# Kernel optimization log

Hardware: AMD Instinct MI355X
Metric: run time of the kernel (lower is better)

The kernel has to match this reference:

```python
import jax, jax.numpy as jnp
import numpy as np

N = 20000      # nodes
E = 320000     # edges (before self loops)
D_IN = 256
D_H = 256
D_E = 8
NEG_SLOPE = 0.2


def setup_inputs() -> dict:
    key = jax.random.key(0)
    ks = jax.random.split(key, 12)
    x = jax.random.normal(ks[0], (N, D_IN), jnp.float32)
    edge_index = jax.random.randint(ks[1], (2, E), 0, N, dtype=jnp.int32)
    edge_attr = jax.random.normal(ks[2], (E, D_E), jnp.float32)
    batch = jnp.zeros((N,), jnp.int32)

    def gat_params(k, d_in):
        k1, k2, k3 = jax.random.split(k, 3)
        W = jax.random.normal(k1, (d_in, D_H), jnp.float32) * (1.0 / np.sqrt(d_in))
        a_s = jax.random.normal(k2, (D_H,), jnp.float32) * 0.1
        a_d = jax.random.normal(k3, (D_H,), jnp.float32) * 0.1
        b = jnp.zeros((D_H,), jnp.float32)
        return W, a_s, a_d, b

    W1, as1, ad1, b1 = gat_params(ks[3], D_IN)
    W2, as2, ad2, b2 = gat_params(ks[4], D_H)
    W3, as3, ad3, b3 = gat_params(ks[5], D_H)
    return dict(x=x, edge_index=edge_index, edge_attr=edge_attr, batch=batch,
                W1=W1, as1=as1, ad1=ad1, b1=b1,
                W2=W2, as2=as2, ad2=ad2, b2=b2,
                W3=W3, as3=as3, ad3=ad3, b3=b3)


def gat_conv(x, src, dst, W, a_src, a_dst, b):
    # PyG GATConv, heads=1: h = x W; alpha_e = leakyrelu(<h_src,a_s> + <h_dst,a_d>)
    h = x @ W                                  # [N, D_H]
    s = h @ a_src                              # [N]
    d = h @ a_dst                              # [N]
    alpha = jax.nn.leaky_relu(s[src] + d[dst], NEG_SLOPE)   # [Etot]
    n = h.shape[0]
    m = jax.ops.segment_max(alpha, dst, num_segments=n)     # per-dst max
    ex = jnp.exp(alpha - m[dst])
    denom = jax.ops.segment_sum(ex, dst, num_segments=n)
    w = ex / (denom[dst] + 1e-16)
    out = jax.ops.segment_sum(h[src] * w[:, None], dst, num_segments=n)
    return out + b


def reference(x, edge_index, edge_attr, batch,
              W1, as1, ad1, b1, W2, as2, ad2, b2, W3, as3, ad3, b3):
    # row-normalize input features (zero norms -> 1e-8)
    norms = jnp.linalg.norm(x, axis=1, keepdims=True)
    norms = jnp.where(norms == 0, 1e-8, norms)
    x = x / norms

    # add self loops once (GATConv default add_self_loops=True);
    # edge_attr is ignored since edge_dim=None in GATConv defaults.
    loop = jnp.arange(N, dtype=edge_index.dtype)
    src = jnp.concatenate([edge_index[0], loop])
    dst = jnp.concatenate([edge_index[1], loop])

    x = jax.nn.gelu(gat_conv(x, src, dst, W1, as1, ad1, b1), approximate=False)
    x = jax.nn.gelu(gat_conv(x, src, dst, W2, as2, ad2, b2), approximate=False)
    x = jax.nn.gelu(gat_conv(x, src, dst, W3, as3, ad3, b3), approximate=False)
    return x
```

## Files before the change

### kernel.cpp

```cpp
#include <hip/hip_runtime.h>
#include <math.h>

#define NN 20000
#define EE 320000
#define DD 256
#define ETOT (EE + NN)
#define EDGE_CAP 1544
#define NCHUNK ((NN + 255) / 256)

typedef __attribute__((ext_vector_type(8))) short bf8;
typedef __attribute__((ext_vector_type(4))) float f32x4;

__device__ __forceinline__ float gelu_exact(float x) {
    return 0.5f * x * (1.0f + erff(x * 0.70710678118654752f));
}

__device__ __forceinline__ unsigned short f2bf(float v) {
    unsigned u = __float_as_uint(v);
    u += 0x7fffu + ((u >> 16) & 1u);
    return (unsigned short)(u >> 16);
}
__device__ __forceinline__ float bf2f(unsigned short h) {
    return __uint_as_float(((unsigned)h) << 16);
}
__device__ __forceinline__ void split2(float v, unsigned short& hi, unsigned short& lo) {
    hi = f2bf(v);
    lo = f2bf(v - bf2f(hi));
}

__global__ __launch_bounds__(256) void norm_k(const float* __restrict__ X,
                                              unsigned short* __restrict__ Xh,
                                              unsigned short* __restrict__ Xl,
                                              float* __restrict__ sdZero,
                                              int* __restrict__ deg) {
    int t = threadIdx.x;
    int bid = blockIdx.x;
    if (t < 24) sdZero[bid * 24 + t] = 0.0f;
    if (t >= 32 && t < 36) deg[bid * 4 + (t - 32)] = 1;

    int wave = (bid * 256 + t) >> 6;
    int lane = t & 63;
    const float4 v = *(const float4*)&X[wave * DD + lane * 4];
    float ss = v.x * v.x + v.y * v.y + v.z * v.z + v.w * v.w;
    for (int off = 32; off > 0; off >>= 1) ss += __shfl_down(ss, off, 64);
    ss = __shfl(ss, 0, 64);
    float n = sqrtf(ss);
    if (n == 0.0f) n = 1e-8f;
    float inv = 1.0f / n;
    float o[4] = {v.x * inv, v.y * inv, v.z * inv, v.w * inv};
    ushort4 hv, lv;
    split2(o[0], hv.x, lv.x);
    split2(o[1], hv.y, lv.y);
    split2(o[2], hv.z, lv.z);
    split2(o[3], hv.w, lv.w);
    *(ushort4*)&Xh[wave * DD + lane * 4] = hv;
    *(ushort4*)&Xl[wave * DD + lane * 4] = lv;
}

__global__ __launch_bounds__(256) void splitw_k(const float* __restrict__ W1, const float* __restrict__ W2,
                                                const float* __restrict__ W3, unsigned short* __restrict__ Whl) {
    __shared__ float tile[64][65];
    int t = threadIdx.x;
    int k0 = blockIdx.x * 64;
    int c0 = blockIdx.y * 64;
    int z = blockIdx.z;
    const float* W = (z == 0) ? W1 : (z == 1) ? W2 : W3;
    unsigned short* Wht = Whl + (size_t)z * 2 * DD * DD;
    unsigned short* Wlt = Wht + DD * DD;
#pragma unroll
    for (int i = 0; i < 16; ++i) {
        int idx = t + i * 256;
        int r = idx >> 6, c = idx & 63;
        tile[r][c] = W[(k0 + r) * DD + c0 + c];
    }
    __syncthreads();
#pragma unroll
    for (int i = 0; i < 16; ++i) {
        int idx = t + i * 256;
        int r = idx >> 6, c = idx & 63;
        float v = tile[c][r];
        unsigned short hi, lo;
        split2(v, hi, lo);
        Wht[(c0 + r) * DD + k0 + c] = hi;
        Wlt[(c0 + r) * DD + k0 + c] = lo;
    }
}

__global__ void count_k(const int* __restrict__ ei, int* deg) {
    int e = blockIdx.x * 256 + threadIdx.x;
    if (e < EE) atomicAdd(&deg[ei[EE + e]], 1);
}

__global__ __launch_bounds__(256) void scanA_k(const int* __restrict__ deg, int* __restrict__ part) {
    __shared__ int red[256];
    int t = threadIdx.x;
    int idx = blockIdx.x * 256 + t;
    red[t] = (idx < NN) ? deg[idx] : 0;
    __syncthreads();
    for (int s = 128; s > 0; s >>= 1) {
        if (t < s) red[t] += red[t + s];
        __syncthreads();
    }
    if (t == 0) part[blockIdx.x] = red[0];
}

__global__ __launch_bounds__(128) void scanB_k(int* __restrict__ part, int* __restrict__ offs) {
    __shared__ int sh[NCHUNK];
    int t = threadIdx.x;
    if (t < NCHUNK) sh[t] = part[t];
    __syncthreads();
    if (t == 0) {
        int run = 0;
        for (int i = 0; i < NCHUNK; ++i) {
            int v = sh[i];
            sh[i] = run;
            run += v;
        }
        offs[NN] = run;
    }
    __syncthreads();
    if (t < NCHUNK) part[t] = sh[t];
}

__global__ __launch_bounds__(256) void scanC_k(const int* __restrict__ deg, const int* __restrict__ part,
                                               int* __restrict__ offs, int* __restrict__ cursor,
                                               int* __restrict__ csr, int* __restrict__ csrD) {
    __shared__ int sh[256];
    int t = threadIdx.x;
    int idx = blockIdx.x * 256 + t;
    int v = (idx < NN) ? deg[idx] : 0;
    sh[t] = v;
    __syncthreads();
    for (int s = 1; s < 256; s <<= 1) {
        int u = (t >= s) ? sh[t - s] : 0;
        __syncthreads();
        sh[t] += u;
        __syncthreads();
    }
    if (idx < NN) {
        int run = part[blockIdx.x] + sh[t] - v;
        offs[idx] = run;
        cursor[idx] = run + 1;
        csr[run] = idx;
        csrD[run] = idx;
    }
}

__global__ void fill_k(const int* __restrict__ ei, int* cursor, int* __restrict__ csr,
                       int* __restrict__ csrD) {
    int e = blockIdx.x * 256 + threadIdx.x;
    if (e < EE) {
        int s = ei[e];
        int d = ei[EE + e];
        int p = atomicAdd(&cursor[d], 1);
        csr[p] = s;
        csrD[p] = d;
    }
}

__global__ __launch_bounds__(256) void alpha_k(const float* __restrict__ sArr,
                                               const float* __restrict__ dArr,
                                               const int* __restrict__ csr,
                                               const int* __restrict__ csrD,
                                               float* __restrict__ wArr) {
    int p = blockIdx.x * 256 + threadIdx.x;
    if (p < ETOT) {
        float a = sArr[csr[p]] + dArr[csrD[p]];
        a = (a > 0.0f) ? a : 0.2f * a;
        wArr[p] = expf(a);
    }
}

#define LDB 36
#define GX ((NN + 63) / 64)
__global__ __launch_bounds__(256) void gemm_sd(const unsigned short* __restrict__ Xh,
                                               const unsigned short* __restrict__ Xl,
                                               const unsigned short* __restrict__ Bh,
                                               const unsigned short* __restrict__ Bl,
                                               const float* __restrict__ a_s,
                                               const float* __restrict__ a_d,
                                               float* __restrict__ H,
                                               float* __restrict__ sArr,
                                               float* __restrict__ dArr) {
    __shared__ unsigned short sBh[2][128 * LDB], sBl[2][128 * LDB];
    int t = threadIdx.x;
    int m0 = blockIdx.x * 64;
    int n0 = blockIdx.y * 128;
    int w = t >> 6, l = t & 63;
    int rofs = l & 15, kch = l >> 4;

    f32x4 acc[8] = {};

    int c1 = t, c2 = t + 256;
    int br1 = c1 >> 2, bo1 = (c1 & 3) * 8;
    int br2 = c2 >> 2, bo2 = (c2 & 3) * 8;
    const unsigned short* Bh1 = &Bh[(n0 + br1) * DD + bo1];
    const unsigned short* Bh2 = &Bh[(n0 + br2) * DD + bo2];
    const unsigned short* Bl1 = &Bl[(n0 + br1) * DD + bo1];
    const unsigned short* Bl2 = &Bl[(n0 + br2) * DD + bo2];
    bf8 rbh1 = *(const bf8*)Bh1;
    bf8 rbh2 = *(const bf8*)Bh2;
    bf8 rbl1 = *(const bf8*)Bl1;
    bf8 rbl2 = *(const bf8*)Bl2;

    int arow = m0 + w * 16 + rofs;
    bool aval = arow < NN;
    const unsigned short* Ahp = &Xh[(size_t)arow * DD + kch * 8];
    const unsigned short* Alp = &Xl[(size_t)arow * DD + kch * 8];
    bf8 zero = {0, 0, 0, 0, 0, 0, 0, 0};
    bf8 ah = aval ? *(const bf8*)Ahp : zero;
    bf8 al = aval ? *(const bf8*)Alp : zero;

    *(bf8*)&sBh[0][br1 * LDB + bo1] = rbh1;
    *(bf8*)&sBh[0][br2 * LDB + bo2] = rbh2;
    *(bf8*)&sBl[0][br1 * LDB + bo1] = rbl1;
    *(bf8*)&sBl[0][br2 * LDB + bo2] = rbl2;
    rbh1 = *(const bf8*)(Bh1 + 32);
    rbh2 = *(const bf8*)(Bh2 + 32);
    rbl1 = *(const bf8*)(Bl1 + 32);
    rbl2 = *(const bf8*)(Bl2 + 32);

#pragma unroll
    for (int kc = 0; kc < 8; ++kc) {
        int cur = kc & 1;
        __syncthreads();
        bf8 nah = zero, nal = zero;
        if (kc < 7) {
            *(bf8*)&sBh[cur ^ 1][br1 * LDB + bo1] = rbh1;
            *(bf8*)&sBh[cur ^ 1][br2 * LDB + bo2] = rbh2;
            *(bf8*)&sBl[cur ^ 1][br1 * LDB + bo1] = rbl1;
            *(bf8*)&sBl[cur ^ 1][br2 * LDB + bo2] = rbl2;
            if (kc < 6) {
                int kn2 = (kc + 2) * 32;
                rbh1 = *(const bf8*)(Bh1 + kn2);
                rbh2 = *(const bf8*)(Bh2 + kn2);
                rbl1 = *(const bf8*)(Bl1 + kn2);
                rbl2 = *(const bf8*)(Bl2 + kn2);
            }
            if (aval) {
                int kn = (kc + 1) * 32;
                nah = *(const bf8*)(Ahp + kn);
                nal = *(const bf8*)(Alp + kn);
            }
        }
#pragma unroll
        for (int nt = 0; nt < 8; ++nt) {
            int r = nt * 16 + rofs;
            bf8 bh = *(const bf8*)&sBh[cur][r * LDB + kch * 8];
            bf8 bl = *(const bf8*)&sBl[cur][r * LDB + kch * 8];
            acc[nt] = __builtin_amdgcn_mfma_f32_16x16x32_bf16(ah, bh, acc[nt], 0, 0, 0);
            acc[nt] = __builtin_amdgcn_mfma_f32_16x16x32_bf16(ah, bl, acc[nt], 0, 0, 0);
            acc[nt] = __builtin_amdgcn_mfma_f32_16x16x32_bf16(al, bh, acc[nt], 0, 0, 0);
        }
        ah = nah;
        al = nal;
    }
    int row0 = m0 + w * 16 + (l >> 4) * 4;
    int colb = l & 15;
    float sp[4] = {0, 0, 0, 0}, dp[4] = {0, 0, 0, 0};
#pragma unroll
    for (int nt = 0; nt < 8; ++nt) {
        int cc = n0 + nt * 16 + colb;
        float vas = a_s[cc], vad = a_d[cc];
#pragma unroll
        for (int r = 0; r < 4; ++r) {
            int row = row0 + r;
            if (row < NN) H[(size_t)row * DD + cc] = acc[nt][r];
            sp[r] += acc[nt][r] * vas;
            dp[r] += acc[nt][r] * vad;
        }
    }
#pragma unroll
    for (int m = 1; m < 16; m <<= 1) {
#pragma unroll
        for (int r = 0; r < 4; ++r) {
            sp[r] += __shfl_xor(sp[r], m, 64);
            dp[r] += __shfl_xor(dp[r], m, 64);
        }
    }
    if (colb == 0) {
#pragma unroll
        for (int r = 0; r < 4; ++r) {
            int row = row0 + r;
            if (row < NN) {
                atomicAdd(&sArr[row], sp[r]);
                atomicAdd(&dArr[row], dp[r]);
            }
        }
    }
}

__global__ __launch_bounds__(256) void spmm_k(const float* __restrict__ H,
                                              const int* __restrict__ offs,
                                              const int* __restrict__ csr,
                                              const float* __restrict__ wArr,
                                              const float* __restrict__ bias,
                                              unsigned short* __restrict__ Oh,
                                              unsigned short* __restrict__ Ol,
                                              float* __restrict__ outf32) {
    __shared__ float wLds[EDGE_CAP];
    __shared__ int sLds[EDGE_CAP];
    int t = threadIdx.x;
    int sub = t & 7;
    int g = t >> 3;
    int dim = blockIdx.x * 32 + sub * 4;
    const float* Hs = H + dim;
    const float4 bvec = *(const float4*)&bias[dim];

    for (int grp = blockIdx.y; grp < NN / 32; grp += (int)gridDim.y) {
        if (grp != (int)blockIdx.y) __syncthreads();
        int dst0 = grp * 32;
        int dst = dst0 + g;
        int blkBeg = offs[dst0];
        int blkEnd = offs[dst0 + 32];
        int base = blkBeg & ~3;
        int cnt = blkEnd - base;
        for (int i = t * 4; i < cnt; i += 1024) {
            *(float4*)&wLds[i] = *(const float4*)&wArr[base + i];
            *(int4*)&sLds[i] = *(const int4*)&csr[base + i];
        }
        int beg = offs[dst], end = offs[dst + 1];
        __syncthreads();

        float den = 0.0f;
        for (int e = beg + sub; e < end; e += 8) den += wLds[e - base];
        den += __shfl_xor(den, 1, 64);
        den += __shfl_xor(den, 2, 64);
        den += __shfl_xor(den, 4, 64);
        float inv = 1.0f / den;

        float4 A0 = make_float4(0, 0, 0, 0), A1 = A0, A2 = A0, A3 = A0;
        int e = beg - base, lend = end - base;
        for (; e + 3 < lend; e += 4) {
            int s0 = sLds[e], s1 = sLds[e + 1], s2 = sLds[e + 2], s3 = sLds[e + 3];
            float w0 = wLds[e], w1 = wLds[e + 1], w2 = wLds[e + 2], w3 = wLds[e + 3];
            const float4 h0 = *(const float4*)&Hs[(size_t)s0 * DD];
            const float4 h1 = *(const float4*)&Hs[(size_t)s1 * DD];
            const float4 h2 = *(const float4*)&Hs[(size_t)s2 * DD];
            const float4 h3 = *(const float4*)&Hs[(size_t)s3 * DD];
            A0.x += w0 * h0.x; A0.y += w0 * h0.y; A0.z += w0 * h0.z; A0.w += w0 * h0.w;
            A1.x += w1 * h1.x; A1.y += w1 * h1.y; A1.z += w1 * h1.z; A1.w += w1 * h1.w;
            A2.x += w2 * h2.x; A2.y += w2 * h2.y; A2.z += w2 * h2.z; A2.w += w2 * h2.w;
            A3.x += w3 * h3.x; A3.y += w3 * h3.y; A3.z += w3 * h3.z; A3.w += w3 * h3.w;
        }
        for (; e < lend; ++e) {
            int s0 = sLds[e];
            float w0 = wLds[e];
            const float4 h0 = *(const float4*)&Hs[(size_t)s0 * DD];
            A0.x += w0 * h0.x; A0.y += w0 * h0.y; A0.z += w0 * h0.z; A0.w += w0 * h0.w;
        }

        float o0 = gelu_exact((A0.x + A1.x + A2.x + A3.x) * inv + bvec.x);
        float o1 = gelu_exact((A0.y + A1.y + A2.y + A3.y) * inv + bvec.y);
        float o2 = gelu_exact((A0.z + A1.z + A2.z + A3.z) * inv + bvec.z);
        float o3 = gelu_exact((A0.w + A1.w + A2.w + A3.w) * inv + bvec.w);

        ushort4 hv, lv;
        split2(o0, hv.x, lv.x);
        split2(o1, hv.y, lv.y);
        split2(o2, hv.z, lv.z);
        split2(o3, hv.w, lv.w);
        *(ushort4*)&Oh[dst * DD + dim] = hv;
        *(ushort4*)&Ol[dst * DD + dim] = lv;
        if (outf32) {
            float4 o = make_float4(o0, o1, o2, o3);
            *(float4*)&outf32[dst * DD + dim] = o;
        }
    }
}

extern "C" void kernel_launch(void* const* d_in, const int* in_sizes, int n_in,
                              void* d_out, int out_size, void* d_ws, size_t ws_size,
                              hipStream_t stream) {
    const float* x  = (const float*)d_in[0];
    const int* ei   = (const int*)d_in[1];
    const float* W1 = (const float*)d_in[4];
    const float* as1 = (const float*)d_in[5];
    const float* ad1 = (const float*)d_in[6];
    const float* b1 = (const float*)d_in[7];
    const float* W2 = (const float*)d_in[8];
    const float* as2 = (const float*)d_in[9];
    const float* ad2 = (const float*)d_in[10];
    const float* b2 = (const float*)d_in[11];
    const float* W3 = (const float*)d_in[12];
    const float* as3 = (const float*)d_in[13];
    const float* ad3 = (const float*)d_in[14];
    const float* b3 = (const float*)d_in[15];

    float* H = (float*)d_ws;
    unsigned short* Xh = (unsigned short*)(H + (size_t)NN * DD);
    unsigned short* Xl = Xh + (size_t)NN * DD;
    unsigned short* Whl = Xl + (size_t)NN * DD;
    float* sd = (float*)(Whl + (size_t)6 * DD * DD);
    int* offs = (int*)(sd + (size_t)6 * NN);
    int* cursor = offs + (NN + 1);
    int* csr = cursor + NN;
    int* deg = csr + ETOT;
    int* csrD = deg + NN;
    float* wArr = (float*)(csrD + ETOT);
    int* part = (int*)(wArr + ETOT);

    float* sA1 = sd,           *dA1 = sd + NN;
    float* sA2 = sd + 2 * NN,  *dA2 = sd + 3 * NN;
    float* sA3 = sd + 4 * NN,  *dA3 = sd + 5 * NN;
    unsigned short* Wt1 = Whl;
    unsigned short* Wt2 = Whl + (size_t)2 * DD * DD;
    unsigned short* Wt3 = Whl + (size_t)4 * DD * DD;

    norm_k<<<NN / 4, 256, 0, stream>>>(x, Xh, Xl, sd, deg);
    count_k<<<(EE + 255) / 256, 256, 0, stream>>>(ei, deg);
    scanA_k<<<NCHUNK, 256, 0, stream>>>(deg, part);
    scanB_k<<<1, 128, 0, stream>>>(part, offs);
    scanC_k<<<NCHUNK, 256, 0, stream>>>(deg, part, offs, cursor, csr, csrD);
    fill_k<<<(EE + 255) / 256, 256, 0, stream>>>(ei, cursor, csr, csrD);
    splitw_k<<<dim3(4, 4, 3), 256, 0, stream>>>(W1, W2, W3, Whl);

    dim3 ggrid(GX, DD / 128);
    dim3 sgrid(DD / 32, 313);
    int agrid = (ETOT + 255) / 256;

    gemm_sd<<<ggrid, 256, 0, stream>>>(Xh, Xl, Wt1, Wt1 + DD * DD, as1, ad1, H, sA1, dA1);
    alpha_k<<<agrid, 256, 0, stream>>>(sA1, dA1, csr, csrD, wArr);
    spmm_k<<<sgrid, 256, 0, stream>>>(H, offs, csr, wArr, b1, Xh, Xl, nullptr);
    gemm_sd<<<ggrid, 256, 0, stream>>>(Xh, Xl, Wt2, Wt2 + DD * DD, as2, ad2, H, sA2, dA2);
    alpha_k<<<agrid, 256, 0, stream>>>(sA2, dA2, csr, csrD, wArr);
    spmm_k<<<sgrid, 256, 0, stream>>>(H, offs, csr, wArr, b2, Xh, Xl, nullptr);
    gemm_sd<<<ggrid, 256, 0, stream>>>(Xh, Xl, Wt3, Wt3 + DD * DD, as3, ad3, H, sA3, dA3);
    alpha_k<<<agrid, 256, 0, stream>>>(sA3, dA3, csr, csrD, wArr);
    spmm_k<<<sgrid, 256, 0, stream>>>(H, offs, csr, wArr, b3, Xh, Xl, (float*)d_out);
}
```

Baseline: 307.4 us.

## Map one wavefront per destination node in SpMM, drop LDS edge staging

The SpMM aggregation kernel is restructured so that each 64-lane wavefront handles one destination node across all 256 feature dims. Edge indices and weights are read straight from global memory, replacing the grid-strided loop over 32-node groups that staged them in LDS behind block barriers. The softmax denominator is accumulated inside the same edge loop. This removes the LDS staging, the barriers and the per-dim-slice redundant reads of edge lists. In exchange, edge-list loads become uniform global loads, and per-wave work now varies with each node's degree.

Result: slower. 353.5 us (+15.0%).

```diff
diff --git a/kernel.cpp b/kernel.cpp
--- a/kernel.cpp
+++ b/kernel.cpp
@@ -5,7 +5,6 @@
 #define EE 320000
 #define DD 256
 #define ETOT (EE + NN)
-#define EDGE_CAP 1544
 #define NCHUNK ((NN + 255) / 256)
 
 typedef __attribute__((ext_vector_type(8))) short bf8;
@@ -298,74 +297,54 @@
                                               unsigned short* __restrict__ Oh,
                                               unsigned short* __restrict__ Ol,
                                               float* __restrict__ outf32) {
-    __shared__ float wLds[EDGE_CAP];
-    __shared__ int sLds[EDGE_CAP];
-    int t = threadIdx.x;
-    int sub = t & 7;
-    int g = t >> 3;
-    int dim = blockIdx.x * 32 + sub * 4;
+    int t = threadIdx.x;
+    int wv = t >> 6, l = t & 63;
+    int dst = blockIdx.x * 4 + wv;
+    int beg = offs[dst], end = offs[dst + 1];
+    int dim = l * 4;
     const float* Hs = H + dim;
+
+    float4 A0 = make_float4(0, 0, 0, 0), A1 = A0, A2 = A0, A3 = A0;
+    float den = 0.0f;
+    int e = beg;
+    for (; e + 3 < end; e += 4) {
+        int s0 = csr[e], s1 = csr[e + 1], s2 = csr[e + 2], s3 = csr[e + 3];
+        float w0 = wArr[e], w1 = wArr[e + 1], w2 = wArr[e + 2], w3 = wArr[e + 3];
+        const float4 h0 = *(const float4*)&Hs[(size_t)s0 * DD];
+        const float4 h1 = *(const float4*)&Hs[(size_t)s1 * DD];
+        const float4 h2 = *(const float4*)&Hs[(size_t)s2 * DD];
+        const float4 h3 = *(const float4*)&Hs[(size_t)s3 * DD];
+        A0.x += w0 * h0.x; A0.y += w0 * h0.y; A0.z += w0 * h0.z; A0.w += w0 * h0.w;
+        A1.x += w1 * h1.x; A1.y += w1 * h1.y; A1.z += w1 * h1.z; A1.w += w1 * h1.w;
+        A2.x += w2 * h2.x; A2.y += w2 * h2.y; A2.z += w2 * h2.z; A2.w += w2 * h2.w;
+        A3.x += w3 * h3.x; A3.y += w3 * h3.y; A3.z += w3 * h3.z; A3.w += w3 * h3.w;
+        den += w0 + w1 + w2 + w3;
+    }
+    for (; e < end; ++e) {
+        int s0 = csr[e];
+        float w0 = wArr[e];
+        const float4 h0 = *(const float4*)&Hs[(size_t)s0 * DD];
+        A0.x += w0 * h0.x; A0.y += w0 * h0.y; A0.z += w0 * h0.z; A0.w += w0 * h0.w;
+        den += w0;
+    }
+
+    float inv = 1.0f / den;
     const float4 bvec = *(const float4*)&bias[dim];
-
-    for (int grp = blockIdx.y; grp < NN / 32; grp += (int)gridDim.y) {
-        if (grp != (int)blockIdx.y) __syncthreads();
-        int dst0 = grp * 32;
-        int dst = dst0 + g;
-        int blkBeg = offs[dst0];
-        int blkEnd = offs[dst0 + 32];
-        int base = blkBeg & ~3;
-        int cnt = blkEnd - base;
-        for (int i = t * 4; i < cnt; i += 1024) {
-            *(float4*)&wLds[i] = *(const float4*)&wArr[base + i];
-            *(int4*)&sLds[i] = *(const int4*)&csr[base + i];
-        }
-        int beg = offs[dst], end = offs[dst + 1];
-        __syncthreads();
-
-        float den = 0.0f;
-        for (int e = beg + sub; e < end; e += 8) den += wLds[e - base];
-        den += __shfl_xor(den, 1, 64);
-        den += __shfl_xor(den, 2, 64);
-        den += __shfl_xor(den, 4, 64);
-        float inv = 1.0f / den;
-
-        float4 A0 = make_float4(0, 0, 0, 0), A1 = A0, A2 = A0, A3 = A0;
-        int e = beg - base, lend = end - base;
-        for (; e + 3 < lend; e += 4) {
-            int s0 = sLds[e], s1 = sLds[e + 1], s2 = sLds[e + 2], s3 = sLds[e + 3];
-            float w0 = wLds[e], w1 = wLds[e + 1], w2 = wLds[e + 2], w3 = wLds[e + 3];
-            const float4 h0 = *(const float4*)&Hs[(size_t)s0 * DD];
-            const float4 h1 = *(const float4*)&Hs[(size_t)s1 * DD];
-            const float4 h2 = *(const float4*)&Hs[(size_t)s2 * DD];
-            const float4 h3 = *(const float4*)&Hs[(size_t)s3 * DD];
-            A0.x += w0 * h0.x; A0.y += w0 * h0.y; A0.z += w0 * h0.z; A0.w += w0 * h0.w;
-            A1.x += w1 * h1.x; A1.y += w1 * h1.y; A1.z += w1 * h1.z; A1.w += w1 * h1.w;
-            A2.x += w2 * h2.x; A2.y += w2 * h2.y; A2.z += w2 * h2.z; A2.w += w2 * h2.w;
-            A3.x += w3 * h3.x; A3.y += w3 * h3.y; A3.z += w3 * h3.z; A3.w += w3 * h3.w;
-        }
-        for (; e < lend; ++e) {
-            int s0 = sLds[e];
-            float w0 = wLds[e];
-            const float4 h0 = *(const float4*)&Hs[(size_t)s0 * DD];
-            A0.x += w0 * h0.x; A0.y += w0 * h0.y; A0.z += w0 * h0.z; A0.w += w0 * h0.w;
-        }
-
-        float o0 = gelu_exact((A0.x + A1.x + A2.x + A3.x) * inv + bvec.x);
-        float o1 = gelu_exact((A0.y + A1.y + A2.y + A3.y) * inv + bvec.y);
-        float o2 = gelu_exact((A0.z + A1.z + A2.z + A3.z) * inv + bvec.z);
-        float o3 = gelu_exact((A0.w + A1.w + A2.w + A3.w) * inv + bvec.w);
-
-        ushort4 hv, lv;
-        split2(o0, hv.x, lv.x);
-        split2(o1, hv.y, lv.y);
-        split2(o2, hv.z, lv.z);
-        split2(o3, hv.w, lv.w);
-        *(ushort4*)&Oh[dst * DD + dim] = hv;
-        *(ushort4*)&Ol[dst * DD + dim] = lv;
-        if (outf32) {
-            float4 o = make_float4(o0, o1, o2, o3);
-            *(float4*)&outf32[dst * DD + dim] = o;
-        }
+    float o0 = gelu_exact((A0.x + A1.x + A2.x + A3.x) * inv + bvec.x);
+    float o1 = gelu_exact((A0.y + A1.y + A2.y + A3.y) * inv + bvec.y);
+    float o2 = gelu_exact((A0.z + A1.z + A2.z + A3.z) * inv + bvec.z);
+    float o3 = gelu_exact((A0.w + A1.w + A2.w + A3.w) * inv + bvec.w);
+
+    ushort4 hv, lv;
+    split2(o0, hv.x, lv.x);
+    split2(o1, hv.y, lv.y);
+    split2(o2, hv.z, lv.z);
+    split2(o3, hv.w, lv.w);
+    *(ushort4*)&Oh[dst * DD + dim] = hv;
+    *(ushort4*)&Ol[dst * DD + dim] = lv;
+    if (outf32) {
+        float4 o = make_float4(o0, o1, o2, o3);
+        *(float4*)&outf32[dst * DD + dim] = o;
     }
 }
 
@@ -416,7 +395,7 @@
     splitw_k<<<dim3(4, 4, 3), 256, 0, stream>>>(W1, W2, W3, Whl);
 
     dim3 ggrid(GX, DD / 128);
-    dim3 sgrid(DD / 32, 313);
+    int sgrid = NN / 4;
     int agrid = (ETOT + 255) / 256;
 
     gemm_sd<<<ggrid, 256, 0, stream>>>(Xh, Xl, Wt1, Wt1 + DD * DD, as1, ad1, H, sA1, dA1);
```

## Preload GEMM A fragments and prefetch second SpMM group's edge data into registers

Applied to the files above, without the earlier changes.

In the GEMM kernel, all eight K-chunks of the A operand (high and low bf16 halves) are now loaded into registers up front instead of being prefetched one chunk ahead. In the SpMM kernel, the grid-stride loop is replaced by a fixed two-group schedule. Each block stages its first group's edge weights and sources into LDS and loads the second group's (blockIdx.y+313) into registers before processing the first, hiding that load latency. This assumes gridDim.y is 313 and the edge count per group fits in two float4 per thread, and the extra register pressure may reduce occupancy.

New measurement: 323.5 us. 5.2% more time.

```diff
diff --git a/kernel.cpp b/kernel.cpp
--- a/kernel.cpp
+++ b/kernel.cpp
@@ -208,8 +208,13 @@
     const unsigned short* Ahp = &Xh[(size_t)arow * DD + kch * 8];
     const unsigned short* Alp = &Xl[(size_t)arow * DD + kch * 8];
     bf8 zero = {0, 0, 0, 0, 0, 0, 0, 0};
-    bf8 ah = aval ? *(const bf8*)Ahp : zero;
-    bf8 al = aval ? *(const bf8*)Alp : zero;
+
+    bf8 Ah[8], Al[8];
+#pragma unroll
+    for (int kc = 0; kc < 8; ++kc) {
+        Ah[kc] = aval ? *(const bf8*)(Ahp + kc * 32) : zero;
+        Al[kc] = aval ? *(const bf8*)(Alp + kc * 32) : zero;
+    }
 
     *(bf8*)&sBh[0][br1 * LDB + bo1] = rbh1;
     *(bf8*)&sBh[0][br2 * LDB + bo2] = rbh2;
@@ -224,7 +229,6 @@
     for (int kc = 0; kc < 8; ++kc) {
         int cur = kc & 1;
         __syncthreads();
-        bf8 nah = zero, nal = zero;
         if (kc < 7) {
             *(bf8*)&sBh[cur ^ 1][br1 * LDB + bo1] = rbh1;
             *(bf8*)&sBh[cur ^ 1][br2 * LDB + bo2] = rbh2;
@@ -237,23 +241,16 @@
                 rbl1 = *(const bf8*)(Bl1 + kn2);
                 rbl2 = *(const bf8*)(Bl2 + kn2);
             }
-            if (aval) {
-                int kn = (kc + 1) * 32;
-                nah = *(const bf8*)(Ahp + kn);
-                nal = *(const bf8*)(Alp + kn);
-            }
         }
 #pragma unroll
         for (int nt = 0; nt < 8; ++nt) {
             int r = nt * 16 + rofs;
             bf8 bh = *(const bf8*)&sBh[cur][r * LDB + kch * 8];
             bf8 bl = *(const bf8*)&sBl[cur][r * LDB + kch * 8];
-            acc[nt] = __builtin_amdgcn_mfma_f32_16x16x32_bf16(ah, bh, acc[nt], 0, 0, 0);
-            acc[nt] = __builtin_amdgcn_mfma_f32_16x16x32_bf16(ah, bl, acc[nt], 0, 0, 0);
-            acc[nt] = __builtin_amdgcn_mfma_f32_16x16x32_bf16(al, bh, acc[nt], 0, 0, 0);
-        }
-        ah = nah;
-        al = nal;
+            acc[nt] = __builtin_amdgcn_mfma_f32_16x16x32_bf16(Ah[kc], bh, acc[nt], 0, 0, 0);
+            acc[nt] = __builtin_amdgcn_mfma_f32_16x16x32_bf16(Ah[kc], bl, acc[nt], 0, 0, 0);
+            acc[nt] = __builtin_amdgcn_mfma_f32_16x16x32_bf16(Al[kc], bh, acc[nt], 0, 0, 0);
+        }
     }
     int row0 = m0 + w * 16 + (l >> 4) * 4;
     int colb = l & 15;
@@ -307,21 +304,9 @@
     const float* Hs = H + dim;
     const float4 bvec = *(const float4*)&bias[dim];
 
-    for (int grp = blockIdx.y; grp < NN / 32; grp += (int)gridDim.y) {
-        if (grp != (int)blockIdx.y) __syncthreads();
-        int dst0 = grp * 32;
+    auto doGroup = [&](int dst0, int base) {
         int dst = dst0 + g;
-        int blkBeg = offs[dst0];
-        int blkEnd = offs[dst0 + 32];
-        int base = blkBeg & ~3;
-        int cnt = blkEnd - base;
-        for (int i = t * 4; i < cnt; i += 1024) {
-            *(float4*)&wLds[i] = *(const float4*)&wArr[base + i];
-            *(int4*)&sLds[i] = *(const int4*)&csr[base + i];
-        }
         int beg = offs[dst], end = offs[dst + 1];
-        __syncthreads();
-
         float den = 0.0f;
         for (int e = beg + sub; e < end; e += 8) den += wLds[e - base];
         den += __shfl_xor(den, 1, 64);
@@ -366,6 +351,38 @@
             float4 o = make_float4(o0, o1, o2, o3);
             *(float4*)&outf32[dst * DD + dim] = o;
         }
+    };
+
+    int g0 = blockIdx.y;
+    int g1 = blockIdx.y + 313;
+    bool has1 = g1 < NN / 32;
+
+    int base0 = offs[g0 * 32] & ~3;
+    int cnt0 = offs[g0 * 32 + 32] - base0;
+    for (int i = t * 4; i < cnt0; i += 1024) {
+        *(float4*)&wLds[i] = *(const float4*)&wArr[base0 + i];
+        *(int4*)&sLds[i] = *(const int4*)&csr[base0 + i];
+    }
+    int base1 = 0, cnt1 = 0;
+    float4 vw0 = make_float4(0, 0, 0, 0), vw1 = make_float4(0, 0, 0, 0);
+    int4 vs0 = make_int4(0, 0, 0, 0), vs1 = make_int4(0, 0, 0, 0);
+    if (has1) {
+        base1 = offs[g1 * 32] & ~3;
+        cnt1 = offs[g1 * 32 + 32] - base1;
+        int i0 = t * 4, i1 = t * 4 + 1024;
+        if (i0 < cnt1) { vw0 = *(const float4*)&wArr[base1 + i0]; vs0 = *(const int4*)&csr[base1 + i0]; }
+        if (i1 < cnt1) { vw1 = *(const float4*)&wArr[base1 + i1]; vs1 = *(const int4*)&csr[base1 + i1]; }
+    }
+    __syncthreads();
+    doGroup(g0 * 32, base0);
+
+    if (has1) {
+        __syncthreads();
+        int i0 = t * 4, i1 = t * 4 + 1024;
+        if (i0 < cnt1) { *(float4*)&wLds[i0] = vw0; *(int4*)&sLds[i0] = vs0; }
+        if (i1 < cnt1) { *(float4*)&wLds[i1] = vw1; *(int4*)&sLds[i1] = vs1; }
+        __syncthreads();
+        doGroup(g1 * 32, base1);
     }
 }
 
```
